# Performance work log

Hardware: AMD Instinct MI355X
Metric: run time of the kernel (lower is better)

The kernel has to match this reference:

```python
import jax, jax.numpy as jnp
import numpy as np

N = 256            # state_space_size
BF = (4, 4, 4)     # branching_factors
T = 128            # time steps
D_IN = 64          # input_size
D_T = 64           # time_embedding_size
BATCH = 16
NUM_NODES = N * 4 * 4 * 4  # 16384


def setup_inputs() -> dict:
    key = jax.random.key(0)
    ks = jax.random.split(key, 20)

    def lin_w(k, out_d, in_d):
        return jax.random.normal(k, (out_d, in_d), jnp.float32) / np.sqrt(in_d)

    inp = {
        "x": jax.random.normal(ks[0], (BATCH, T, N), jnp.float32),
        "t_embeddings_schedule": jax.random.normal(ks[1], (T, D_T), jnp.float32),
        "input_vector": jax.random.normal(ks[2], (BATCH, T, D_IN), jnp.float32),
        # Fanout node params
        "Wa": lin_w(ks[3], NUM_NODES, N),
        "ba": jnp.zeros((NUM_NODES,), jnp.float32),
        "Wt": lin_w(ks[4], NUM_NODES, D_T),
        "Wi": lin_w(ks[5], NUM_NODES, D_IN),
        # Node with bf[:3]=[4,4,4]: reduces last 4 -> [N,4,4]
        "w3": jax.random.normal(ks[6], (N, 4, 4, 4), jnp.float32) * np.sqrt(2.0 / (4 + N * 16)),
        "tW3": lin_w(ks[7], N * 16, D_T),
        "tb3": jnp.zeros((N * 16,), jnp.float32),
        # Node with bf[:2]=[4,4]
        "w2": jax.random.normal(ks[8], (N, 4, 4), jnp.float32) * np.sqrt(2.0 / (4 + N * 4)),
        "tW2": lin_w(ks[9], N * 4, D_T),
        "tb2": jnp.zeros((N * 4,), jnp.float32),
        # Node with bf[:1]=[4]
        "w1": jax.random.normal(ks[10], (N, 4), jnp.float32) * np.sqrt(2.0 / (4 + N)),
        "tW1": lin_w(ks[11], N, D_T),
        "tb1": jnp.zeros((N,), jnp.float32),
    }
    return inp


def _node(act, t_emb, w, tW, tb):
    # act: [..., T, N, *bf]; w: [N, *bf]; reduce last branching dim
    tproj = (t_emb @ tW.T + tb).reshape(t_emb.shape[0], *w.shape[:-1])  # [T, N, *bf[:-1]]
    pre = (w * act).sum(-1) + tproj  # broadcast over leading batch dims
    return jax.nn.softplus(pre)


def reference(x, t_embeddings_schedule, input_vector, Wa, ba, Wt, Wi,
              w3, tW3, tb3, w2, tW2, tb2, w1, tW1, tb1):
    t_emb = t_embeddings_schedule
    # Fanout: [B, T, N] -> [B, T, N, 4, 4, 4]
    pre = x @ Wa.T + ba + (t_emb @ Wt.T) + input_vector @ Wi.T  # [B, T, NUM_NODES]
    act = jax.nn.softplus(pre.reshape(*pre.shape[:-1], N, *BF))
    # Tree: deepest node first (insert-at-1 order in original)
    act = _node(act, t_emb, w3, tW3, tb3)  # [B, T, N, 4, 4]
    act = _node(act, t_emb, w2, tW2, tb2)  # [B, T, N, 4]
    act = _node(act, t_emb, w1, tW1, tb1)  # [B, T, N]
    return act
```

## Files before the change

kernel.cpp:

```cpp
#include <hip/hip_runtime.h>

typedef __attribute__((ext_vector_type(4))) float f32x4;
typedef __attribute__((ext_vector_type(8))) __bf16 bf16x8;
typedef __attribute__((ext_vector_type(8))) unsigned short u16x8;

__device__ __forceinline__ unsigned short f2bf(float f) {
    unsigned int u = __float_as_uint(f);
    u += 0x7fffu + ((u >> 16) & 1u);
    return (unsigned short)(u >> 16);
}

__device__ __forceinline__ float softplus_f(float x) {
    float e = __expf(-fabsf(x));
    return fmaxf(x, 0.0f) + __logf(1.0f + e);
}

typedef __attribute__((address_space(3))) void lds_void_t;
typedef __attribute__((address_space(1))) void glb_void_t;

__device__ __forceinline__ void load16_to_lds(const void* g, const void* l) {
    __builtin_amdgcn_global_load_lds((glb_void_t*)(unsigned long long)g,
                                     (lds_void_t*)(unsigned int)(unsigned long long)l,
                                     16, 0, 0);
}

#define REPACK_NB 4
#define REPACK_BLOCKS 864
__global__ __launch_bounds__(256) void repack(
        const float* __restrict__ x, const float* __restrict__ iv,
        const float* __restrict__ temb,
        const float* __restrict__ Wa, const float* __restrict__ Wi,
        const float* __restrict__ Wt,
        unsigned short* __restrict__ Abf ) {
    const int stride = REPACK_BLOCKS * 256;
    const int tid0 = blockIdx.x * 256 + threadIdx.x;
    float4 f[REPACK_NB][2];
    #pragma unroll
    for (int c = 0; c < REPACK_NB; ++c) {
        const int idx = tid0 + c * stride;
        const bool isA = idx < 98304;
        const int widx = isA ? idx : idx - 98304;
        const int row = widx / 48;
        const int kk  = (widx % 48) * 8;
        const float* p0 = isA ? (x    + (size_t)row * 256) : (Wa + (size_t)row * 256);
        const float* p1 = isA ? (iv   + (size_t)row * 64)  : (Wi + (size_t)row * 64);
        const float* p2 = isA ? (temb + (size_t)(row & 127) * 64) : (Wt + (size_t)row * 64);
        const float* src = (kk < 256) ? (p0 + kk) : ((kk < 320) ? (p1 + kk - 256) : (p2 + kk - 320));
        f[c][0] = ((const float4*)src)[0];
        f[c][1] = ((const float4*)src)[1];
    }
    #pragma unroll
    for (int c = 0; c < REPACK_NB; ++c) {
        const int idx = tid0 + c * stride;
        u16x8 o;
        o[0] = f2bf(f[c][0].x); o[1] = f2bf(f[c][0].y); o[2] = f2bf(f[c][0].z); o[3] = f2bf(f[c][0].w);
        o[4] = f2bf(f[c][1].x); o[5] = f2bf(f[c][1].y); o[6] = f2bf(f[c][1].z); o[7] = f2bf(f[c][1].w);
        *(u16x8*)(Abf + (size_t)idx * 8) = o;
    }
}

__global__ __launch_bounds__(256) void tproj(
        const float* __restrict__ temb,
        const float* __restrict__ tW3, const float* __restrict__ tb3,
        const float* __restrict__ tW2, const float* __restrict__ tb2,
        const float* __restrict__ tW1, const float* __restrict__ tb1,
        float* __restrict__ tp3T, float* __restrict__ tp2T, float* __restrict__ tp1T) {
    __shared__ float se[32 * 64];
    const int tid = threadIdx.x;
    const int tbase = blockIdx.y * 32;
    for (int i = tid; i < 32 * 64; i += 256) se[i] = temb[tbase * 64 + i];
    __syncthreads();
    const int j = blockIdx.x * 64 + (tid >> 2);
    const float* W; const float* bias; float* outp; int jl;
    if      (j < 4096) { W = tW3; bias = tb3; outp = tp3T; jl = j; }
    else if (j < 5120) { W = tW2; bias = tb2; outp = tp2T; jl = j - 4096; }
    else               { W = tW1; bias = tb1; outp = tp1T; jl = j - 5120; }
    float4 wreg[16];
    const float4* wrow = (const float4*)(W + (size_t)jl * 64);
    #pragma unroll
    for (int k = 0; k < 16; ++k) wreg[k] = wrow[k];
    const float b = bias[jl];
    #pragma unroll
    for (int s = 0; s < 8; ++s) {
        const int tl = (tid & 3) + s * 4;
        const float4* e4 = (const float4*)&se[tl * 64];
        float a = b;
        #pragma unroll
        for (int k = 0; k < 16; ++k) {
            float4 e = e4[k];
            a += wreg[k].x * e.x + wreg[k].y * e.y + wreg[k].z * e.z + wreg[k].w * e.w;
        }
        outp[(size_t)jl * 128 + tbase + tl] = a;
    }
}

__global__ __launch_bounds__(256, 3)
void fused_gemm_tree(const unsigned short* __restrict__ Wbf,
                     const unsigned short* __restrict__ Abf,
                     const float* __restrict__ ba,
                     const float* __restrict__ tp3T, const float* __restrict__ tp2T,
                     const float* __restrict__ tp1T,
                     const float* __restrict__ w3, const float* __restrict__ w2,
                     const float* __restrict__ w1,
                     float* __restrict__ out) {
    __shared__ unsigned short sW[128 * 64];
    __shared__ unsigned short sA[128 * 64];

    const int tid  = threadIdx.x;
    const int wave = tid >> 6;
    const int lane = tid & 63;
    const int wr = wave >> 1;
    const int wc = wave & 1;
    const int lane15 = lane & 15;
    const int quad = lane >> 4;

    const int node0 = blockIdx.x * 128;
    const int m0    = blockIdx.y * 128;

    f32x4 acc[4][4];
    const f32x4 zero = {0.0f, 0.0f, 0.0f, 0.0f};
    #pragma unroll
    for (int i = 0; i < 4; ++i)
        #pragma unroll
        for (int j = 0; j < 4; ++j) acc[i][j] = zero;

    const int wrow = wr * 64 + lane15;
    const int arow = wc * 64 + lane15;
    const int swz  = lane15 & 7;

    const unsigned short* aBase = Wbf + (size_t)node0 * 384;
    const unsigned short* bBase = Abf + (size_t)m0 * 384;

    for (int k0 = 0; k0 < 384; k0 += 64) {
        __syncthreads();
        #pragma unroll
        for (int rr = 0; rr < 4; ++rr) {
            const int p = rr * 256 + tid;
            const int row = p >> 3;
            const int kchunk = (p & 7) ^ (row & 7);
            const size_t soff = (size_t)row * 384 + k0 + kchunk * 8;
            load16_to_lds(aBase + soff, &sW[(size_t)(rr * 256 + wave * 64) * 8]);
            load16_to_lds(bBase + soff, &sA[(size_t)(rr * 256 + wave * 64) * 8]);
        }
        __syncthreads();

        #pragma unroll
        for (int s = 0; s < 2; ++s) {
            const int cpos = ((s * 4 + quad) ^ swz) * 8;
            bf16x8 af[4], bfr[4];
            #pragma unroll
            for (int i = 0; i < 4; ++i) af[i]  = *(const bf16x8*)&sW[(wrow + i * 16) * 64 + cpos];
            #pragma unroll
            for (int j = 0; j < 4; ++j) bfr[j] = *(const bf16x8*)&sA[(arow + j * 16) * 64 + cpos];
            #pragma unroll
            for (int i = 0; i < 4; ++i)
                #pragma unroll
                for (int j = 0; j < 4; ++j)
                    acc[i][j] = __builtin_amdgcn_mfma_f32_16x16x32_bf16(af[i], bfr[j], acc[i][j], 0, 0, 0);
        }
    }

    const int n = blockIdx.x * 2 + wr;

    float bav[4][4], w3v[4][4], w2v[4], w1v[4];
    #pragma unroll
    for (int i = 0; i < 4; ++i) {
        #pragma unroll
        for (int r = 0; r < 4; ++r) {
            const int nl = i * 16 + quad * 4 + r;
            bav[i][r] = ba[node0 + wr * 64 + nl];
            w3v[i][r] = w3[n * 64 + nl];
        }
        w2v[i] = w2[n * 16 + i * 4 + quad];
        w1v[i] = w1[n * 4 + i];
    }

    const int tbase = wc * 64 + lane15;
    float s1[4] = {0.0f, 0.0f, 0.0f, 0.0f};

    #pragma unroll
    for (int i = 0; i < 4; ++i) {
        const float* tp3row = tp3T + (size_t)(n * 16 + i * 4 + quad) * 128;
        const float* tp2row = tp2T + (size_t)(n * 4 + i) * 128;
        #pragma unroll
        for (int j = 0; j < 4; ++j) {
            const int t = tbase + j * 16;
            float p3 = 0.0f;
            #pragma unroll
            for (int r = 0; r < 4; ++r) {
                float a0 = softplus_f(acc[i][j][r] + bav[i][r]);
                p3 = fmaf(a0, w3v[i][r], p3);
            }
            float a3 = softplus_f(p3 + tp3row[t]);
            float c2 = a3 * w2v[i];
            c2 += __shfl_xor(c2, 16);
            c2 += __shfl_xor(c2, 32);
            float a2 = softplus_f(c2 + tp2row[t]);
            s1[j] = fmaf(a2, w1v[i], s1[j]);
        }
    }
    #pragma unroll
    for (int j = 0; j < 4; ++j) {
        const int t = tbase + j * 16;
        float o = softplus_f(s1[j] + tp1T[(size_t)n * 128 + t]);
        if (quad == 0) out[(size_t)(m0 + t) * 256 + n] = o;
    }
}

extern "C" void kernel_launch(void* const* d_in, const int* in_sizes, int n_in,
                              void* d_out, int out_size, void* d_ws, size_t ws_size,
                              hipStream_t stream) {
    const float* x    = (const float*)d_in[0];
    const float* temb = (const float*)d_in[1];
    const float* iv   = (const float*)d_in[2];
    const float* Wa   = (const float*)d_in[3];
    const float* ba   = (const float*)d_in[4];
    const float* Wt   = (const float*)d_in[5];
    const float* Wi   = (const float*)d_in[6];
    const float* w3   = (const float*)d_in[7];
    const float* tW3  = (const float*)d_in[8];
    const float* tb3  = (const float*)d_in[9];
    const float* w2   = (const float*)d_in[10];
    const float* tW2  = (const float*)d_in[11];
    const float* tb2  = (const float*)d_in[12];
    const float* w1   = (const float*)d_in[13];
    const float* tW1  = (const float*)d_in[14];
    const float* tb1  = (const float*)d_in[15];
    float* out = (float*)d_out;

    char* ws = (char*)d_ws;
    unsigned short* Abf = (unsigned short*)(ws);
    unsigned short* Wbf = (unsigned short*)(ws + 1572864);
    float* tp3T = (float*)(ws + 14155776);
    float* tp2T = (float*)(ws + 16252928);
    float* tp1T = (float*)(ws + 16777216);

    repack<<<dim3(REPACK_BLOCKS), dim3(256), 0, stream>>>(x, iv, temb, Wa, Wi, Wt, Abf);
    tproj<<<dim3(84, 4), dim3(256), 0, stream>>>(temb, tW3, tb3, tW2, tb2, tW1, tb1,
                                                 tp3T, tp2T, tp1T);
    fused_gemm_tree<<<dim3(128, 16), dim3(256), 0, stream>>>(Wbf, Abf, ba, tp3T, tp2T, tp1T,
                                                             w3, w2, w1, out);
}
```

Baseline: 158.7 us.

## Switch GEMM to 32x32x16 MFMA and restructure fused tree epilogue

Replaces the 16x16x32 bf16 MFMA tiling (4x4 fragments per wave) with 32x32x16 MFMA (2x2 fragments), which changes the LDS fragment loads and the accumulator layout. The tree-reduction epilogue is rewritten to match the new layout. Bias and w3 are read as float4, the tp3/tp2/tp1 projections are preloaded, and reductions now need a single cross-half shuffle with every lane storing output. The repack kernel launches twice the blocks with half the work per thread. The larger MFMA should cut LDS read traffic and instruction count, at the cost of a different register and bank-access pattern.

```diff
diff --git a/kernel.cpp b/kernel.cpp
--- a/kernel.cpp
+++ b/kernel.cpp
@@ -1,6 +1,6 @@
 #include <hip/hip_runtime.h>
 
-typedef __attribute__((ext_vector_type(4))) float f32x4;
+typedef __attribute__((ext_vector_type(16))) float f32x16;
 typedef __attribute__((ext_vector_type(8))) __bf16 bf16x8;
 typedef __attribute__((ext_vector_type(8))) unsigned short u16x8;
 
@@ -24,8 +24,8 @@
                                      16, 0, 0);
 }
 
-#define REPACK_NB 4
-#define REPACK_BLOCKS 864
+#define REPACK_NB 2
+#define REPACK_BLOCKS 1728
 __global__ __launch_bounds__(256) void repack(
         const float* __restrict__ x, const float* __restrict__ iv,
         const float* __restrict__ temb,
@@ -111,25 +111,25 @@
     const int lane = tid & 63;
     const int wr = wave >> 1;
     const int wc = wave & 1;
-    const int lane15 = lane & 15;
-    const int quad = lane >> 4;
+    const int lane31 = lane & 31;
+    const int h = lane >> 5;
 
     const int node0 = blockIdx.x * 128;
     const int m0    = blockIdx.y * 128;
 
-    f32x4 acc[4][4];
-    const f32x4 zero = {0.0f, 0.0f, 0.0f, 0.0f};
-    #pragma unroll
-    for (int i = 0; i < 4; ++i)
-        #pragma unroll
-        for (int j = 0; j < 4; ++j) acc[i][j] = zero;
-
-    const int wrow = wr * 64 + lane15;
-    const int arow = wc * 64 + lane15;
-    const int swz  = lane15 & 7;
+    f32x16 acc[2][2];
+    #pragma unroll
+    for (int fm = 0; fm < 2; ++fm)
+        #pragma unroll
+        for (int cf = 0; cf < 2; ++cf)
+            #pragma unroll
+            for (int r = 0; r < 16; ++r) acc[fm][cf][r] = 0.0f;
 
     const unsigned short* aBase = Wbf + (size_t)node0 * 384;
     const unsigned short* bBase = Abf + (size_t)m0 * 384;
+
+    const int wrow0 = wr * 64 + lane31;
+    const int arow0 = wc * 64 + lane31;
 
     for (int k0 = 0; k0 < 384; k0 += 64) {
         __syncthreads();
@@ -145,65 +145,99 @@
         __syncthreads();
 
         #pragma unroll
-        for (int s = 0; s < 2; ++s) {
-            const int cpos = ((s * 4 + quad) ^ swz) * 8;
-            bf16x8 af[4], bfr[4];
-            #pragma unroll
-            for (int i = 0; i < 4; ++i) af[i]  = *(const bf16x8*)&sW[(wrow + i * 16) * 64 + cpos];
-            #pragma unroll
-            for (int j = 0; j < 4; ++j) bfr[j] = *(const bf16x8*)&sA[(arow + j * 16) * 64 + cpos];
-            #pragma unroll
-            for (int i = 0; i < 4; ++i)
+        for (int s = 0; s < 4; ++s) {
+            const int kc = s * 2 + h;
+            bf16x8 af[2], bf[2];
+            #pragma unroll
+            for (int fm = 0; fm < 2; ++fm) {
+                const int row = wrow0 + fm * 32;
+                af[fm] = *(const bf16x8*)&sW[row * 64 + (kc ^ (row & 7)) * 8];
+            }
+            #pragma unroll
+            for (int cf = 0; cf < 2; ++cf) {
+                const int row = arow0 + cf * 32;
+                bf[cf] = *(const bf16x8*)&sA[row * 64 + (kc ^ (row & 7)) * 8];
+            }
+            #pragma unroll
+            for (int fm = 0; fm < 2; ++fm)
                 #pragma unroll
-                for (int j = 0; j < 4; ++j)
-                    acc[i][j] = __builtin_amdgcn_mfma_f32_16x16x32_bf16(af[i], bfr[j], acc[i][j], 0, 0, 0);
+                for (int cf = 0; cf < 2; ++cf)
+                    acc[fm][cf] = __builtin_amdgcn_mfma_f32_32x32x16_bf16(af[fm], bf[cf], acc[fm][cf], 0, 0, 0);
         }
     }
 
     const int n = blockIdx.x * 2 + wr;
-
-    float bav[4][4], w3v[4][4], w2v[4], w1v[4];
+    const int t0 = wc * 64 + lane31;
+
+    float4 bav[2][4], w3v[2][4];
+    #pragma unroll
+    for (int fm = 0; fm < 2; ++fm)
+        #pragma unroll
+        for (int s2 = 0; s2 < 4; ++s2) {
+            const int leafbase = fm * 32 + 8 * s2 + 4 * h;
+            bav[fm][s2] = *(const float4*)&ba[node0 + wr * 64 + leafbase];
+            w3v[fm][s2] = *(const float4*)&w3[n * 64 + leafbase];
+        }
+    float w2v[4][2], w1v[4];
     #pragma unroll
     for (int i = 0; i < 4; ++i) {
         #pragma unroll
-        for (int r = 0; r < 4; ++r) {
-            const int nl = i * 16 + quad * 4 + r;
-            bav[i][r] = ba[node0 + wr * 64 + nl];
-            w3v[i][r] = w3[n * 64 + nl];
-        }
-        w2v[i] = w2[n * 16 + i * 4 + quad];
+        for (int s2b = 0; s2b < 2; ++s2b)
+            w2v[i][s2b] = w2[n * 16 + i * 4 + 2 * s2b + h];
         w1v[i] = w1[n * 4 + i];
     }
-
-    const int tbase = wc * 64 + lane15;
-    float s1[4] = {0.0f, 0.0f, 0.0f, 0.0f};
-
-    #pragma unroll
-    for (int i = 0; i < 4; ++i) {
-        const float* tp3row = tp3T + (size_t)(n * 16 + i * 4 + quad) * 128;
-        const float* tp2row = tp2T + (size_t)(n * 4 + i) * 128;
-        #pragma unroll
-        for (int j = 0; j < 4; ++j) {
-            const int t = tbase + j * 16;
-            float p3 = 0.0f;
-            #pragma unroll
-            for (int r = 0; r < 4; ++r) {
-                float a0 = softplus_f(acc[i][j][r] + bav[i][r]);
-                p3 = fmaf(a0, w3v[i][r], p3);
-            }
-            float a3 = softplus_f(p3 + tp3row[t]);
-            float c2 = a3 * w2v[i];
-            c2 += __shfl_xor(c2, 16);
-            c2 += __shfl_xor(c2, 32);
-            float a2 = softplus_f(c2 + tp2row[t]);
-            s1[j] = fmaf(a2, w1v[i], s1[j]);
-        }
-    }
-    #pragma unroll
-    for (int j = 0; j < 4; ++j) {
-        const int t = tbase + j * 16;
-        float o = softplus_f(s1[j] + tp1T[(size_t)n * 128 + t]);
-        if (quad == 0) out[(size_t)(m0 + t) * 256 + n] = o;
+    float tp3v[2][2][4], tp2v[2][2][2], tp1v[2];
+    #pragma unroll
+    for (int fm = 0; fm < 2; ++fm)
+        #pragma unroll
+        for (int cf = 0; cf < 2; ++cf) {
+            const int t = t0 + cf * 32;
+            #pragma unroll
+            for (int s2 = 0; s2 < 4; ++s2) {
+                const int i  = fm * 2 + (s2 >> 1);
+                const int jj = 2 * (s2 & 1) + h;
+                tp3v[fm][cf][s2] = tp3T[(size_t)((n * 4 + i) * 4 + jj) * 128 + t];
+            }
+            #pragma unroll
+            for (int b = 0; b < 2; ++b)
+                tp2v[fm][cf][b] = tp2T[(size_t)(n * 4 + fm * 2 + b) * 128 + t];
+        }
+    #pragma unroll
+    for (int cf = 0; cf < 2; ++cf) tp1v[cf] = tp1T[(size_t)n * 128 + t0 + cf * 32];
+
+    float s1[2] = {0.0f, 0.0f};
+    #pragma unroll
+    for (int fm = 0; fm < 2; ++fm) {
+        #pragma unroll
+        for (int cf = 0; cf < 2; ++cf) {
+            #pragma unroll
+            for (int b = 0; b < 2; ++b) {
+                float cs = 0.0f;
+                #pragma unroll
+                for (int s2b = 0; s2b < 2; ++s2b) {
+                    const int s2 = 2 * b + s2b;
+                    float p3 = 0.0f;
+                    const float* bv = (const float*)&bav[fm][s2];
+                    const float* wv = (const float*)&w3v[fm][s2];
+                    #pragma unroll
+                    for (int l = 0; l < 4; ++l) {
+                        float a0 = softplus_f(acc[fm][cf][s2 * 4 + l] + bv[l]);
+                        p3 = fmaf(a0, wv[l], p3);
+                    }
+                    float a3 = softplus_f(p3 + tp3v[fm][cf][s2]);
+                    cs = fmaf(a3, w2v[fm * 2 + b][s2b], cs);
+                }
+                float Q = cs + __shfl_xor(cs, 32);
+                float a2 = softplus_f(Q + tp2v[fm][cf][b]);
+                s1[cf] = fmaf(a2, w1v[fm * 2 + b], s1[cf]);
+            }
+        }
+    }
+    {
+        const float sj = h ? s1[1] : s1[0];
+        const float tq = h ? tp1v[1] : tp1v[0];
+        const int t = t0 + h * 32;
+        out[(size_t)(m0 + t) * 256 + n] = softplus_f(sj + tq);
     }
 }
 
```

After: 155.8 us. No clear change (-1.8%).
